# Kernel optimization log

Measured on AMD Instinct MI355X. Metric: run time of the kernel, lower is better.

The kernel has to match this reference:

```python
import jax, jax.numpy as jnp
import numpy as np

E, TOPK, HID, FFN = 8, 2, 1024, 2048  # experts, top_k, hidden K, intermediate N
B, S = 2, 1024


def setup_inputs() -> dict:
    key = jax.random.key(0)
    ks = jax.random.split(key, 7)
    return {
        "x": jax.random.normal(ks[0], (B, S, HID), jnp.float32),
        "router_weight": jax.random.normal(ks[1], (E, HID), jnp.float32) * 0.02,
        "router_bias": jax.random.normal(ks[2], (E,), jnp.float32) * 0.02,
        "w1": jax.random.normal(ks[3], (E, 2 * FFN, HID), jnp.float32) * 0.02,  # [E,2N,K] gate|up
        "w1_bias": jax.random.normal(ks[4], (E, 2 * FFN), jnp.float32) * 0.02,
        "w2": jax.random.normal(ks[5], (E, HID, FFN), jnp.float32) * 0.02,      # [E,K,N]
        "w2_bias": jax.random.normal(ks[6], (E, HID), jnp.float32) * 0.02,
        "top_k": TOPK,
    }


def reference(x, router_weight, router_bias, w1, w1_bias, w2, w2_bias, top_k):
    Bb, Ss, K = x.shape
    xf = x.reshape(-1, K)                                   # [M,K]
    M = xf.shape[0]
    Ne = w1.shape[0]
    # --- route_tokens: softmax over experts, then top-k (megablocks style) ---
    logits = xf @ router_weight.T + router_bias             # [M,E]
    probs = jax.nn.softmax(logits, axis=-1)
    topk_w, topk_ids = jax.lax.top_k(probs, top_k)          # [M,topk]
    # combine weights: scatter top-k probs into dense [M,E]
    comb = jnp.zeros((M, Ne), xf.dtype).at[jnp.arange(M)[:, None], topk_ids].add(topk_w)
    # --- fused experts (dense combine formulation, same math as grouped GEMM) ---
    gu = jnp.einsum('mk,enk->men', xf, w1) + w1_bias[None]  # [M,E,2N]
    Nf = gu.shape[-1] // 2
    gate, up = gu[..., :Nf], gu[..., Nf:]
    h = jax.nn.silu(gate) * up                              # silu_and_mul (SwiGLU)
    down = jnp.einsum('men,ekn->mek', h, w2) + w2_bias[None]  # [M,E,K]
    out = jnp.einsum('mek,me->mk', down, comb)              # weighted combine
    return out.reshape(Bb, Ss, K), topk_w
```

## Files before the change

kernel.cpp:

```cpp
#include <hip/hip_runtime.h>
#include <hip/hip_bf16.h>
#include <math.h>

#define E_    8
#define HID_  1024
#define FFN_  2048
#define M_    2048
#define NP_   (M_*2)

typedef __attribute__((ext_vector_type(8))) short bf16x8;
typedef __attribute__((ext_vector_type(8))) short short8v;
typedef __attribute__((ext_vector_type(4))) float f32x4;
typedef __attribute__((ext_vector_type(4))) int   i32x4;

typedef const __attribute__((address_space(1))) void GVOID;
typedef __attribute__((address_space(3))) void LVOID;

#define VMCNT4 asm volatile("s_waitcnt vmcnt(4)" ::: "memory")
#define VMCNT0 asm volatile("s_waitcnt vmcnt(0)" ::: "memory")

__device__ __forceinline__ short f2bf(float f) {
    union { __hip_bfloat16 b; short s; } u;
    u.b = __float2bfloat16(f);
    return u.s;
}

__device__ __forceinline__ bf16x8 pk8(f32x4 lo, f32x4 hi) {
    unsigned u0, u1, u2, u3;
    asm("v_cvt_pk_bf16_f32 %0, %1, %2" : "=v"(u0) : "v"(lo.x), "v"(lo.y));
    asm("v_cvt_pk_bf16_f32 %0, %1, %2" : "=v"(u1) : "v"(lo.z), "v"(lo.w));
    asm("v_cvt_pk_bf16_f32 %0, %1, %2" : "=v"(u2) : "v"(hi.x), "v"(hi.y));
    asm("v_cvt_pk_bf16_f32 %0, %1, %2" : "=v"(u3) : "v"(hi.z), "v"(hi.w));
    union { i32x4 i; bf16x8 b; } r;
    r.i = (i32x4){(int)u0, (int)u1, (int)u2, (int)u3};
    return r.b;
}

__global__ __launch_bounds__(64) void router_kernel(
    const float* __restrict__ x, const float* __restrict__ rw,
    const float* __restrict__ rb, int* __restrict__ ids,
    float* __restrict__ wts, int* __restrict__ cnt,
    float* __restrict__ topk_out, __hip_bfloat16* __restrict__ xb)
{
    const int m    = blockIdx.x;
    const int lane = threadIdx.x;
    const float4* xm4 = (const float4*)(x + (size_t)m * HID_);

    float4 xv[4];
#pragma unroll
    for (int j = 0; j < 4; ++j) xv[j] = xm4[j*64 + lane];

    short4* xbr = (short4*)(xb + (size_t)m * HID_);
#pragma unroll
    for (int j = 0; j < 4; ++j) {
        short4 o;
        o.x = f2bf(xv[j].x); o.y = f2bf(xv[j].y);
        o.z = f2bf(xv[j].z); o.w = f2bf(xv[j].w);
        xbr[j*64 + lane] = o;
    }

    float lg[E_];
#pragma unroll
    for (int e = 0; e < E_; ++e) {
        const float4* we4 = (const float4*)(rw + e * HID_);
        float s = 0.f;
#pragma unroll
        for (int j = 0; j < 4; ++j) {
            float4 w = we4[j*64 + lane];
            s = fmaf(xv[j].x, w.x, s);
            s = fmaf(xv[j].y, w.y, s);
            s = fmaf(xv[j].z, w.z, s);
            s = fmaf(xv[j].w, w.w, s);
        }
        lg[e] = s;
    }
#pragma unroll
    for (int off = 32; off; off >>= 1)
#pragma unroll
        for (int e = 0; e < E_; ++e) lg[e] += __shfl_xor(lg[e], off);

    if (lane == 0) {
        float l2[E_], p[E_];
        float mx = -1e30f;
#pragma unroll
        for (int e = 0; e < E_; ++e) { l2[e] = lg[e] + rb[e]; mx = fmaxf(mx, l2[e]); }
        float sum = 0.f;
#pragma unroll
        for (int e = 0; e < E_; ++e) { p[e] = expf(l2[e] - mx); sum += p[e]; }
        float inv = 1.f / sum;
#pragma unroll
        for (int e = 0; e < E_; ++e) p[e] *= inv;

        int   i1 = -1, i2 = -1;
        float v1 = -1e30f, v2 = -1e30f;
#pragma unroll
        for (int e = 0; e < E_; ++e) {
            float pe = p[e];
            if (pe > v1)      { v2 = v1; i2 = i1; v1 = pe; i1 = e; }
            else if (pe > v2) { v2 = pe; i2 = e; }
        }
        ids[2*m]   = i1;  ids[2*m+1]   = i2;
        wts[2*m]   = v1;  wts[2*m+1]   = v2;
        topk_out[2*m]   = v1;
        topk_out[2*m+1] = v2;
        atomicAdd(&cnt[i1], 1);
        atomicAdd(&cnt[i2], 1);
    }
}

__global__ void offsets_kernel(const int* __restrict__ cnt,
                               int* __restrict__ off, int* __restrict__ fill)
{
    if (threadIdx.x == 0 && blockIdx.x == 0) {
        int acc = 0;
        for (int e = 0; e < E_; ++e) { off[e] = acc; fill[e] = acc; acc += cnt[e]; }
    }
}

__global__ __launch_bounds__(256) void scatter_kernel(
    const int* __restrict__ ids, const float* __restrict__ wts,
    int* __restrict__ fill, int* __restrict__ gtok, float* __restrict__ gwt,
    int* __restrict__ pos)
{
    int m = blockIdx.x * 256 + threadIdx.x;
    if (m >= M_) return;
#pragma unroll
    for (int s = 0; s < 2; ++s) {
        int e = ids[2*m + s];
        int p = atomicAdd(&fill[e], 1);
        gtok[p] = m;
        gwt[p]  = wts[2*m + s];
        pos[2*m + s] = p;
    }
}

__global__ __launch_bounds__(256, 3) void gemm1_kernel(
    const __hip_bfloat16* __restrict__ xb, const float* __restrict__ w1,
    const float* __restrict__ w1b, const int* __restrict__ gtok,
    const int* __restrict__ cnt, const int* __restrict__ off,
    __hip_bfloat16* __restrict__ h,
    const float* __restrict__ w2, __hip_bfloat16* __restrict__ w2bf)
{
    if (blockIdx.z == 8) {
        int pb = blockIdx.x + 32 * blockIdx.y;
        const float4* src = (const float4*)w2;
        short8v* dst = (short8v*)w2bf;
        size_t cb0 = (size_t)pb * 4096;
        for (int it = 0; it < 4; ++it) {
            size_t cbase = cb0 + it*1024;
            float4 a[4], b[4];
#pragma unroll
            for (int u = 0; u < 4; ++u) {
                size_t c = cbase + u*256 + threadIdx.x;
                a[u] = src[2*c];
                b[u] = src[2*c + 1];
            }
#pragma unroll
            for (int u = 0; u < 4; ++u) {
                size_t c = cbase + u*256 + threadIdx.x;
                short8v o;
                o[0] = f2bf(a[u].x); o[1] = f2bf(a[u].y);
                o[2] = f2bf(a[u].z); o[3] = f2bf(a[u].w);
                o[4] = f2bf(b[u].x); o[5] = f2bf(b[u].y);
                o[6] = f2bf(b[u].z); o[7] = f2bf(b[u].w);
                dst[c] = o;
            }
        }
        return;
    }

    const int e  = blockIdx.z;
    const int ce = cnt[e];
    const int t0 = blockIdx.y * 128;
    if (t0 >= ce) return;
    const int n0   = blockIdx.x * 64;
    const int base = off[e];
    const float* w1e = w1 + (size_t)e * (2*FFN_) * HID_;

    __shared__ __align__(16) __hip_bfloat16 As[2][128*32];
    __shared__ __align__(16) float          Bsf[2][128*32];

    const int tid  = threadIdx.x;
    const int lane = tid & 63;
    const int wid  = tid >> 6;
    const int wm   = wid >> 1;
    const int wn   = wid & 1;
    const int cf   = lane >> 4;

    const __hip_bfloat16* asrc[2];
#pragma unroll
    for (int q = 0; q < 2; ++q) {
        int slot = q*256 + tid;
        int r = slot >> 2, p = slot & 3;
        int c = p ^ ((r >> 1) & 3);
        int rr  = min(t0 + r, ce - 1);
        asrc[q] = xb + (size_t)gtok[base + rr] * HID_ + c*8;
    }
    const float* bsrc[4];
#pragma unroll
    for (int q = 0; q < 4; ++q) {
        int slot = q*256 + tid;
        int r = slot >> 3, p = slot & 7;
        int c = p ^ (r & 7);
        int q2 = r >> 5, s = r & 31;
        int grow = (q2 & 1) ? (FFN_ + n0 + (q2>>1)*32 + s)
                            : (       n0 + (q2>>1)*32 + s);
        bsrc[q] = w1e + (size_t)grow * HID_ + c*4;
    }

    auto STAGE = [&](int b, int k0) {
#pragma unroll
        for (int q = 0; q < 2; ++q)
            __builtin_amdgcn_global_load_lds((GVOID*)(asrc[q] + k0),
                (LVOID*)(&As[b][(q*256 + wid*64)*8]), 16, 0, 0);
#pragma unroll
        for (int q = 0; q < 4; ++q)
            __builtin_amdgcn_global_load_lds((GVOID*)(bsrc[q] + k0),
                (LVOID*)(&Bsf[b][(q*256 + wid*64)*4]), 16, 0, 0);
    };

    f32x4 acc[4][4];
#pragma unroll
    for (int m = 0; m < 4; ++m)
#pragma unroll
        for (int n = 0; n < 4; ++n) acc[m][n] = (f32x4){0.f,0.f,0.f,0.f};

    auto COMPUTE = [&](int cb) {
        bf16x8 af[4], bfr[4];
#pragma unroll
        for (int m = 0; m < 4; ++m) {
            int r = wm*64 + m*16 + (lane & 15);
            int sw = cf ^ ((r >> 1) & 3);
            af[m] = *(bf16x8*)&As[cb][r*32 + sw*8];
        }
#pragma unroll
        for (int n = 0; n < 4; ++n) {
            int r = wn*64 + n*16 + (lane & 15);
            int p0 = (2*cf)     ^ (r & 7);
            int p1 = (2*cf + 1) ^ (r & 7);
            f32x4 lo = *(f32x4*)&Bsf[cb][r*32 + p0*4];
            f32x4 hi = *(f32x4*)&Bsf[cb][r*32 + p1*4];
            bfr[n] = pk8(lo, hi);
        }
        __builtin_amdgcn_s_setprio(1);
#pragma unroll
        for (int m = 0; m < 4; ++m)
#pragma unroll
            for (int n = 0; n < 4; ++n)
                acc[m][n] = __builtin_amdgcn_mfma_f32_16x16x32_bf16(
                    af[m], bfr[n], acc[m][n], 0, 0, 0);
        __builtin_amdgcn_s_setprio(0);
    };

    const int NT = HID_/32;
    STAGE(0, 0);
    __syncthreads();
    for (int t = 0; t < NT; ++t) {
        int cur = t & 1, nxt = cur ^ 1;
        if (t + 1 < NT) STAGE(nxt, (t+1)*32);
        COMPUTE(cur);
        __syncthreads();
    }

    const float* w1be = w1b + e*2*FFN_;
#pragma unroll
    for (int n = 0; n < 2; ++n) {
        int col = n0 + wn*32 + n*16 + (lane & 15);
        float bg = w1be[col];
        float bu = w1be[FFN_ + col];
#pragma unroll
        for (int m = 0; m < 4; ++m) {
            int rb2 = t0 + wm*64 + m*16 + (lane >> 4)*4;
#pragma unroll
            for (int i = 0; i < 4; ++i) {
                int t = rb2 + i;
                if (t < ce) {
                    float g = acc[m][n][i]   + bg;
                    float u = acc[m][n+2][i] + bu;
                    float hv = (g / (1.f + __expf(-g))) * u;
                    h[(size_t)(base + t)*FFN_ + col] = __float2bfloat16(hv);
                }
            }
        }
    }
}

__global__ __launch_bounds__(256, 3) void gemm2_kernel(
    const __hip_bfloat16* __restrict__ h, const __hip_bfloat16* __restrict__ w2bf,
    const float* __restrict__ w2b, const float* __restrict__ gwt,
    const int* __restrict__ cnt, const int* __restrict__ off,
    float* __restrict__ dpair)
{
    const int e  = blockIdx.z & 7;
    const int ks = blockIdx.z >> 3;
    const int ce = cnt[e];
    const int t0 = blockIdx.y * 128;
    if (t0 >= ce) return;
    const int n0    = blockIdx.x * 128;
    const int base  = off[e];
    const int kbase = ks * (FFN_/2);
    const __hip_bfloat16* w2e = w2bf + (size_t)e * HID_ * FFN_;

    __shared__ __align__(16) __hip_bfloat16 As[3][128*32];
    __shared__ __align__(16) __hip_bfloat16 Bs[3][128*32];

    const int tid  = threadIdx.x;
    const int lane = tid & 63;
    const int wid  = tid >> 6;
    const int wm   = wid >> 1;
    const int wn   = wid & 1;

    const __hip_bfloat16 *asrc[2], *bsrc[2];
#pragma unroll
    for (int q = 0; q < 2; ++q) {
        int slot = q*256 + tid;
        int r = slot >> 2, p = slot & 3;
        int c = p ^ ((r >> 1) & 3);
        int rr = min(t0 + r, ce - 1);
        asrc[q] = h   + (size_t)(base + rr) * FFN_ + kbase + c*8;
        bsrc[q] = w2e + (size_t)(n0 + r)    * FFN_ + kbase + c*8;
    }

    auto STAGE = [&](int b, int k0) {
#pragma unroll
        for (int q = 0; q < 2; ++q)
            __builtin_amdgcn_global_load_lds((GVOID*)(asrc[q] + k0),
                (LVOID*)(&As[b][(q*256 + wid*64)*8]), 16, 0, 0);
#pragma unroll
        for (int q = 0; q < 2; ++q)
            __builtin_amdgcn_global_load_lds((GVOID*)(bsrc[q] + k0),
                (LVOID*)(&Bs[b][(q*256 + wid*64)*8]), 16, 0, 0);
    };

    f32x4 acc[4][4];
#pragma unroll
    for (int m = 0; m < 4; ++m)
#pragma unroll
        for (int n = 0; n < 4; ++n) acc[m][n] = (f32x4){0.f,0.f,0.f,0.f};

    const int cf = lane >> 4;
    auto COMPUTE = [&](int cb) {
        bf16x8 af[4], bfr[4];
#pragma unroll
        for (int m = 0; m < 4; ++m) {
            int r = wm*64 + m*16 + (lane & 15);
            int sw = cf ^ ((r >> 1) & 3);
            af[m] = *(bf16x8*)&As[cb][r*32 + sw*8];
        }
#pragma unroll
        for (int n = 0; n < 4; ++n) {
            int r = wn*64 + n*16 + (lane & 15);
            int sw = cf ^ ((r >> 1) & 3);
            bfr[n] = *(bf16x8*)&Bs[cb][r*32 + sw*8];
        }
        __builtin_amdgcn_s_setprio(1);
#pragma unroll
        for (int m = 0; m < 4; ++m)
#pragma unroll
            for (int n = 0; n < 4; ++n)
                acc[m][n] = __builtin_amdgcn_mfma_f32_16x16x32_bf16(
                    af[m], bfr[n], acc[m][n], 0, 0, 0);
        __builtin_amdgcn_s_setprio(0);
    };

    const int NT = (FFN_/2)/32;
    STAGE(0, 0);
    STAGE(1, 32);
    VMCNT4;
    __builtin_amdgcn_s_barrier();

    int cb = 0;
    for (int t = 0; t < NT-2; ++t) {
        int sb = cb + 2; if (sb >= 3) sb -= 3;
        STAGE(sb, (t+2)*32);
        COMPUTE(cb);
        VMCNT4;
        __builtin_amdgcn_s_barrier();
        if (++cb == 3) cb = 0;
    }
    COMPUTE(cb);
    VMCNT0;
    __builtin_amdgcn_s_barrier();
    if (++cb == 3) cb = 0;
    COMPUTE(cb);

    const float* w2be = w2b + e*HID_;
    float* dpk = dpair + (size_t)ks * NP_ * HID_;
#pragma unroll
    for (int n = 0; n < 4; ++n) {
        int col = n0 + wn*64 + n*16 + (lane & 15);
        float bias = (ks == 0) ? w2be[col] : 0.f;
#pragma unroll
        for (int m = 0; m < 4; ++m) {
            int rb2 = t0 + wm*64 + m*16 + (lane >> 4)*4;
#pragma unroll
            for (int i = 0; i < 4; ++i) {
                int t = rb2 + i;
                if (t < ce) {
                    int p   = base + t;
                    float w = gwt[p];
                    dpk[(size_t)p*HID_ + col] = w * (acc[m][n][i] + bias);
                }
            }
        }
    }
}

__global__ __launch_bounds__(256) void combine_kernel(
    const float* __restrict__ dpair, const int* __restrict__ pos,
    float* __restrict__ out)
{
    int idx = blockIdx.x * 256 + threadIdx.x;
    int m   = idx >> 8;
    int c4  = (idx & 255) * 4;
    int p0 = pos[2*m], p1 = pos[2*m+1];
    const float* d0 = dpair;
    const float* d1 = dpair + (size_t)NP_ * HID_;
    float4 a0 = *(const float4*)(d0 + (size_t)p0*HID_ + c4);
    float4 a1 = *(const float4*)(d1 + (size_t)p0*HID_ + c4);
    float4 b0 = *(const float4*)(d0 + (size_t)p1*HID_ + c4);
    float4 b1 = *(const float4*)(d1 + (size_t)p1*HID_ + c4);
    float4 o = make_float4((a0.x+a1.x)+(b0.x+b1.x), (a0.y+a1.y)+(b0.y+b1.y),
                           (a0.z+a1.z)+(b0.z+b1.z), (a0.w+a1.w)+(b0.w+b1.w));
    *(float4*)(out + (size_t)m*HID_ + c4) = o;
}

__global__ __launch_bounds__(256) void gemm1_rs_kernel(
    const __hip_bfloat16* __restrict__ xb, const float* __restrict__ w1,
    const float* __restrict__ w1b, const int* __restrict__ gtok,
    const int* __restrict__ cnt, const int* __restrict__ off,
    __hip_bfloat16* __restrict__ h)
{
    const int e  = blockIdx.z;
    const int ce = cnt[e];
    const int t0 = blockIdx.y * 128;
    if (t0 >= ce) return;
    const int n0   = blockIdx.x * 64;
    const int base = off[e];
    const float* w1e = w1 + (size_t)e * (2*FFN_) * HID_;

    __shared__ __align__(16) __hip_bfloat16 As[128*64];
    __shared__ __align__(16) __hip_bfloat16 Bs[128*64];

    const int tid  = threadIdx.x;
    const int lane = tid & 63;
    const int wid  = tid >> 6;
    const int wm   = wid >> 1;
    const int wn   = wid & 1;

    const __hip_bfloat16* asrc[4];
#pragma unroll
    for (int q = 0; q < 4; ++q) {
        int slot = q*256 + tid;
        int r = slot >> 3, p = slot & 7;
        int rr  = min(t0 + r, ce - 1);
        int tok = gtok[base + rr];
        int c = p ^ (r & 7);
        asrc[q] = xb + (size_t)tok * HID_ + c*8;
    }

    const int brow = tid >> 1;
    const int hk   = tid & 1;
    const int q2 = brow >> 5, s = brow & 31;
    const int grow = (q2 & 1) ? (FFN_ + n0 + (q2>>1)*32 + s)
                              : (       n0 + (q2>>1)*32 + s);
    const float* bsrc = w1e + (size_t)grow * HID_ + hk*32;

    f32x4 acc[4][4];
#pragma unroll
    for (int m = 0; m < 4; ++m)
#pragma unroll
        for (int n = 0; n < 4; ++n) acc[m][n] = (f32x4){0.f,0.f,0.f,0.f};

    float4 breg[8];
#pragma unroll
    for (int j = 0; j < 8; ++j) breg[j] = *(const float4*)(bsrc + j*4);

    for (int k0 = 0; k0 < HID_; k0 += 64) {
#pragma unroll
        for (int q = 0; q < 4; ++q) {
            __builtin_amdgcn_global_load_lds(
                (GVOID*)(asrc[q] + k0),
                (LVOID*)(&As[(q*256 + wid*64)*8]), 16, 0, 0);
        }
#pragma unroll
        for (int cc = 0; cc < 4; ++cc) {
            union { bf16x8 v; short s8[8]; } u;
            const float* f0 = (const float*)&breg[2*cc];
#pragma unroll
            for (int j = 0; j < 8; ++j) u.s8[j] = f2bf(f0[j]);
            int c = hk*4 + cc, p = c ^ (brow & 7);
            *(bf16x8*)&Bs[brow*64 + p*8] = u.v;
        }
        __syncthreads();

        if (k0 + 64 < HID_) {
#pragma unroll
            for (int j = 0; j < 8; ++j) breg[j] = *(const float4*)(bsrc + (k0+64) + j*4);
        }

        bf16x8 af[4][2], bfr[4][2];
#pragma unroll
        for (int m = 0; m < 4; ++m)
#pragma unroll
            for (int kk = 0; kk < 2; ++kk) {
                int r = wm*64 + m*16 + (lane & 15);
                int c = kk*4 + (lane >> 4), p = c ^ (r & 7);
                af[m][kk] = *(bf16x8*)&As[r*64 + p*8];
            }
#pragma unroll
        for (int n = 0; n < 4; ++n)
#pragma unroll
            for (int kk = 0; kk < 2; ++kk) {
                int r = wn*64 + n*16 + (lane & 15);
                int c = kk*4 + (lane >> 4), p = c ^ (r & 7);
                bfr[n][kk] = *(bf16x8*)&Bs[r*64 + p*8];
            }
#pragma unroll
        for (int kk = 0; kk < 2; ++kk)
#pragma unroll
            for (int m = 0; m < 4; ++m)
#pragma unroll
                for (int n = 0; n < 4; ++n)
                    acc[m][n] = __builtin_amdgcn_mfma_f32_16x16x32_bf16(
                        af[m][kk], bfr[n][kk], acc[m][n], 0, 0, 0);
        __syncthreads();
    }

    const float* w1be = w1b + e*2*FFN_;
#pragma unroll
    for (int n = 0; n < 2; ++n) {
        int col = n0 + wn*32 + n*16 + (lane & 15);
        float bg = w1be[col];
        float bu = w1be[FFN_ + col];
#pragma unroll
        for (int m = 0; m < 4; ++m) {
            int rb2 = t0 + wm*64 + m*16 + (lane >> 4)*4;
#pragma unroll
            for (int i = 0; i < 4; ++i) {
                int t = rb2 + i;
                if (t < ce) {
                    float g = acc[m][n][i]   + bg;
                    float u = acc[m][n+2][i] + bu;
                    float hv = (g / (1.f + __expf(-g))) * u;
                    h[(size_t)(base + t)*FFN_ + col] = __float2bfloat16(hv);
                }
            }
        }
    }
}

__global__ __launch_bounds__(256) void gemm2_rs_kernel(
    const __hip_bfloat16* __restrict__ h, const float* __restrict__ w2,
    const float* __restrict__ w2b, const int* __restrict__ gtok,
    const float* __restrict__ gwt, const int* __restrict__ cnt,
    const int* __restrict__ off, float* __restrict__ out)
{
    const int e  = blockIdx.z;
    const int ce = cnt[e];
    const int t0 = blockIdx.y * 128;
    if (t0 >= ce) return;
    const int n0   = blockIdx.x * 128;
    const int base = off[e];
    const float* w2e = w2 + (size_t)e * HID_ * FFN_;

    __shared__ __align__(16) __hip_bfloat16 As[128*64];
    __shared__ __align__(16) __hip_bfloat16 Bs[128*64];

    const int tid  = threadIdx.x;
    const int lane = tid & 63;
    const int wid  = tid >> 6;
    const int wm   = wid >> 1;
    const int wn   = wid & 1;

    const __hip_bfloat16* asrc[4];
#pragma unroll
    for (int q = 0; q < 4; ++q) {
        int slot = q*256 + tid;
        int r = slot >> 3, p = slot & 7;
        int rr = min(t0 + r, ce - 1);
        int c = p ^ (r & 7);
        asrc[q] = h + (size_t)(base + rr) * FFN_ + c*8;
    }

    const int brow = tid >> 1;
    const int hk   = tid & 1;
    const float* bsrc = w2e + (size_t)(n0 + brow) * FFN_ + hk*32;

    f32x4 acc[4][4];
#pragma unroll
    for (int m = 0; m < 4; ++m)
#pragma unroll
        for (int n = 0; n < 4; ++n) acc[m][n] = (f32x4){0.f,0.f,0.f,0.f};

    float4 breg[8];
#pragma unroll
    for (int j = 0; j < 8; ++j) breg[j] = *(const float4*)(bsrc + j*4);

    for (int k0 = 0; k0 < FFN_; k0 += 64) {
#pragma unroll
        for (int q = 0; q < 4; ++q) {
            __builtin_amdgcn_global_load_lds(
                (GVOID*)(asrc[q] + k0),
                (LVOID*)(&As[(q*256 + wid*64)*8]), 16, 0, 0);
        }
#pragma unroll
        for (int cc = 0; cc < 4; ++cc) {
            union { bf16x8 v; short s8[8]; } u;
            const float* f0 = (const float*)&breg[2*cc];
#pragma unroll
            for (int j = 0; j < 8; ++j) u.s8[j] = f2bf(f0[j]);
            int c = hk*4 + cc, p = c ^ (brow & 7);
            *(bf16x8*)&Bs[brow*64 + p*8] = u.v;
        }
        __syncthreads();

        if (k0 + 64 < FFN_) {
#pragma unroll
            for (int j = 0; j < 8; ++j) breg[j] = *(const float4*)(bsrc + (k0+64) + j*4);
        }

        bf16x8 af[4][2], bfr[4][2];
#pragma unroll
        for (int m = 0; m < 4; ++m)
#pragma unroll
            for (int kk = 0; kk < 2; ++kk) {
                int r = wm*64 + m*16 + (lane & 15);
                int c = kk*4 + (lane >> 4), p = c ^ (r & 7);
                af[m][kk] = *(bf16x8*)&As[r*64 + p*8];
            }
#pragma unroll
        for (int n = 0; n < 4; ++n)
#pragma unroll
            for (int kk = 0; kk < 2; ++kk) {
                int r = wn*64 + n*16 + (lane & 15);
                int c = kk*4 + (lane >> 4), p = c ^ (r & 7);
                bfr[n][kk] = *(bf16x8*)&Bs[r*64 + p*8];
            }
#pragma unroll
        for (int kk = 0; kk < 2; ++kk)
#pragma unroll
            for (int m = 0; m < 4; ++m)
#pragma unroll
                for (int n = 0; n < 4; ++n)
                    acc[m][n] = __builtin_amdgcn_mfma_f32_16x16x32_bf16(
                        af[m][kk], bfr[n][kk], acc[m][n], 0, 0, 0);
        __syncthreads();
    }

    const float* w2be = w2b + e*HID_;
#pragma unroll
    for (int n = 0; n < 4; ++n) {
        int col = n0 + wn*64 + n*16 + (lane & 15);
        float bias = w2be[col];
#pragma unroll
        for (int m = 0; m < 4; ++m) {
            int rb2 = t0 + wm*64 + m*16 + (lane >> 4)*4;
#pragma unroll
            for (int i = 0; i < 4; ++i) {
                int t = rb2 + i;
                if (t < ce) {
                    int p   = base + t;
                    float w = gwt[p];
                    atomicAdd(&out[(size_t)gtok[p]*HID_ + col], w * (acc[m][n][i] + bias));
                }
            }
        }
    }
}

extern "C" void kernel_launch(void* const* d_in, const int* in_sizes, int n_in,
                              void* d_out, int out_size, void* d_ws, size_t ws_size,
                              hipStream_t stream)
{
    const float* x   = (const float*)d_in[0];
    const float* rw  = (const float*)d_in[1];
    const float* rb  = (const float*)d_in[2];
    const float* w1  = (const float*)d_in[3];
    const float* w1b = (const float*)d_in[4];
    const float* w2  = (const float*)d_in[5];
    const float* w2b = (const float*)d_in[6];

    float* out      = (float*)d_out;
    float* topk_out = out + (size_t)M_ * HID_;

    char*  ws   = (char*)d_ws;
    int*   ids  = (int*)  (ws);
    float* wts  = (float*)(ws + 16384);
    int*   gtok = (int*)  (ws + 32768);
    float* gwt  = (float*)(ws + 49152);
    int*   cnt  = (int*)  (ws + 65536);
    int*   off  = (int*)  (ws + 65536 + 128);
    int*   fill = (int*)  (ws + 65536 + 256);
    int*   pos  = (int*)  (ws + 98304);

    const size_t MB = 1024*1024;
    __hip_bfloat16* xb    = (__hip_bfloat16*)(ws + 131072);
    __hip_bfloat16* h     = (__hip_bfloat16*)(ws + 131072 + 4*MB);
    float*          dpair = (float*)         (ws + 131072 + 20*MB);
    __hip_bfloat16* w2bf  = (__hip_bfloat16*)(ws + 131072 + 52*MB);
    const bool tier2 = (ws_size >= 131072 + 84*MB);

    hipMemsetAsync(cnt, 0, E_ * sizeof(int), stream);

    router_kernel<<<M_, 64, 0, stream>>>(x, rw, rb, ids, wts, cnt, topk_out, xb);
    offsets_kernel<<<1, 64, 0, stream>>>(cnt, off, fill);
    scatter_kernel<<<M_/256, 256, 0, stream>>>(ids, wts, fill, gtok, gwt, pos);

    if (tier2) {
        dim3 g1(FFN_/64, M_/128, E_ + 1);
        gemm1_kernel<<<g1, 256, 0, stream>>>(xb, w1, w1b, gtok, cnt, off, h,
                                             w2, w2bf);

        dim3 g2(HID_/128, M_/128, 2*E_);
        gemm2_kernel<<<g2, 256, 0, stream>>>(h, w2bf, w2b, gwt, cnt, off, dpair);

        combine_kernel<<<(M_*HID_)/(256*4), 256, 0, stream>>>(dpair, pos, out);
    } else {
        hipMemsetAsync(out, 0, (size_t)M_ * HID_ * sizeof(float), stream);

        dim3 g1(FFN_/64, M_/128, E_);
        gemm1_rs_kernel<<<g1, 256, 0, stream>>>(xb, w1, w1b, gtok, cnt, off, h);

        dim3 g2(HID_/128, M_/128, E_);
        gemm2_rs_kernel<<<g2, 256, 0, stream>>>(h, w2, w2b, gtok, gwt, cnt, off, out);
    }
}
```

Baseline: 229.4 us.

## Use fixed per-expert slot regions and fuse token scatter into router

Each expert now gets a fixed region of M slots, so token positions are assigned directly in the router with atomics on per-expert fill counters. This removes the separate offsets and scatter kernels and their launch overhead. The cost is larger h and dpair buffers, indexed by expert*M, and a much higher workspace requirement for the fast tier2 path. If the workspace is too small, execution falls back to the slower path.

```diff
diff --git a/kernel.cpp b/kernel.cpp
--- a/kernel.cpp
+++ b/kernel.cpp
@@ -6,7 +6,7 @@
 #define HID_  1024
 #define FFN_  2048
 #define M_    2048
-#define NP_   (M_*2)
+#define NP2_  (E_*M_)
 
 typedef __attribute__((ext_vector_type(8))) short bf16x8;
 typedef __attribute__((ext_vector_type(8))) short short8v;
@@ -38,8 +38,8 @@
 
 __global__ __launch_bounds__(64) void router_kernel(
     const float* __restrict__ x, const float* __restrict__ rw,
-    const float* __restrict__ rb, int* __restrict__ ids,
-    float* __restrict__ wts, int* __restrict__ cnt,
+    const float* __restrict__ rb, int* __restrict__ fill,
+    int* __restrict__ gtok, float* __restrict__ gwt, int* __restrict__ pos,
     float* __restrict__ topk_out, __hip_bfloat16* __restrict__ xb)
 {
     const int m    = blockIdx.x;
@@ -99,46 +99,21 @@
             if (pe > v1)      { v2 = v1; i2 = i1; v1 = pe; i1 = e; }
             else if (pe > v2) { v2 = pe; i2 = e; }
         }
-        ids[2*m]   = i1;  ids[2*m+1]   = i2;
-        wts[2*m]   = v1;  wts[2*m+1]   = v2;
         topk_out[2*m]   = v1;
         topk_out[2*m+1] = v2;
-        atomicAdd(&cnt[i1], 1);
-        atomicAdd(&cnt[i2], 1);
-    }
-}
-
-__global__ void offsets_kernel(const int* __restrict__ cnt,
-                               int* __restrict__ off, int* __restrict__ fill)
-{
-    if (threadIdx.x == 0 && blockIdx.x == 0) {
-        int acc = 0;
-        for (int e = 0; e < E_; ++e) { off[e] = acc; fill[e] = acc; acc += cnt[e]; }
-    }
-}
-
-__global__ __launch_bounds__(256) void scatter_kernel(
-    const int* __restrict__ ids, const float* __restrict__ wts,
-    int* __restrict__ fill, int* __restrict__ gtok, float* __restrict__ gwt,
-    int* __restrict__ pos)
-{
-    int m = blockIdx.x * 256 + threadIdx.x;
-    if (m >= M_) return;
-#pragma unroll
-    for (int s = 0; s < 2; ++s) {
-        int e = ids[2*m + s];
-        int p = atomicAdd(&fill[e], 1);
-        gtok[p] = m;
-        gwt[p]  = wts[2*m + s];
-        pos[2*m + s] = p;
+        int p1s = atomicAdd(&fill[i1], 1);
+        int s1  = i1*M_ + p1s;
+        gtok[s1] = m; gwt[s1] = v1; pos[2*m]   = s1;
+        int p2s = atomicAdd(&fill[i2], 1);
+        int s2  = i2*M_ + p2s;
+        gtok[s2] = m; gwt[s2] = v2; pos[2*m+1] = s2;
     }
 }
 
 __global__ __launch_bounds__(256, 3) void gemm1_kernel(
     const __hip_bfloat16* __restrict__ xb, const float* __restrict__ w1,
     const float* __restrict__ w1b, const int* __restrict__ gtok,
-    const int* __restrict__ cnt, const int* __restrict__ off,
-    __hip_bfloat16* __restrict__ h,
+    const int* __restrict__ fill, __hip_bfloat16* __restrict__ h,
     const float* __restrict__ w2, __hip_bfloat16* __restrict__ w2bf)
 {
     if (blockIdx.z == 8) {
@@ -170,11 +145,11 @@
     }
 
     const int e  = blockIdx.z;
-    const int ce = cnt[e];
+    const int ce = fill[e];
     const int t0 = blockIdx.y * 128;
     if (t0 >= ce) return;
     const int n0   = blockIdx.x * 64;
-    const int base = off[e];
+    const int base = e * M_;
     const float* w1e = w1 + (size_t)e * (2*FFN_) * HID_;
 
     __shared__ __align__(16) __hip_bfloat16 As[2][128*32];
@@ -288,16 +263,15 @@
 __global__ __launch_bounds__(256, 3) void gemm2_kernel(
     const __hip_bfloat16* __restrict__ h, const __hip_bfloat16* __restrict__ w2bf,
     const float* __restrict__ w2b, const float* __restrict__ gwt,
-    const int* __restrict__ cnt, const int* __restrict__ off,
-    float* __restrict__ dpair)
+    const int* __restrict__ fill, float* __restrict__ dpair)
 {
     const int e  = blockIdx.z & 7;
     const int ks = blockIdx.z >> 3;
-    const int ce = cnt[e];
+    const int ce = fill[e];
     const int t0 = blockIdx.y * 128;
     if (t0 >= ce) return;
     const int n0    = blockIdx.x * 128;
-    const int base  = off[e];
+    const int base  = e * M_;
     const int kbase = ks * (FFN_/2);
     const __hip_bfloat16* w2e = w2bf + (size_t)e * HID_ * FFN_;
 
@@ -385,7 +359,7 @@
     COMPUTE(cb);
 
     const float* w2be = w2b + e*HID_;
-    float* dpk = dpair + (size_t)ks * NP_ * HID_;
+    float* dpk = dpair + (size_t)ks * NP2_ * HID_;
 #pragma unroll
     for (int n = 0; n < 4; ++n) {
         int col = n0 + wn*64 + n*16 + (lane & 15);
@@ -415,7 +389,7 @@
     int c4  = (idx & 255) * 4;
     int p0 = pos[2*m], p1 = pos[2*m+1];
     const float* d0 = dpair;
-    const float* d1 = dpair + (size_t)NP_ * HID_;
+    const float* d1 = dpair + (size_t)NP2_ * HID_;
     float4 a0 = *(const float4*)(d0 + (size_t)p0*HID_ + c4);
     float4 a1 = *(const float4*)(d1 + (size_t)p0*HID_ + c4);
     float4 b0 = *(const float4*)(d0 + (size_t)p1*HID_ + c4);
@@ -428,15 +402,14 @@
 __global__ __launch_bounds__(256) void gemm1_rs_kernel(
     const __hip_bfloat16* __restrict__ xb, const float* __restrict__ w1,
     const float* __restrict__ w1b, const int* __restrict__ gtok,
-    const int* __restrict__ cnt, const int* __restrict__ off,
-    __hip_bfloat16* __restrict__ h)
+    const int* __restrict__ fill, __hip_bfloat16* __restrict__ h)
 {
     const int e  = blockIdx.z;
-    const int ce = cnt[e];
+    const int ce = fill[e];
     const int t0 = blockIdx.y * 128;
     if (t0 >= ce) return;
     const int n0   = blockIdx.x * 64;
-    const int base = off[e];
+    const int base = e * M_;
     const float* w1e = w1 + (size_t)e * (2*FFN_) * HID_;
 
     __shared__ __align__(16) __hip_bfloat16 As[128*64];
@@ -553,15 +526,15 @@
 __global__ __launch_bounds__(256) void gemm2_rs_kernel(
     const __hip_bfloat16* __restrict__ h, const float* __restrict__ w2,
     const float* __restrict__ w2b, const int* __restrict__ gtok,
-    const float* __restrict__ gwt, const int* __restrict__ cnt,
-    const int* __restrict__ off, float* __restrict__ out)
+    const float* __restrict__ gwt, const int* __restrict__ fill,
+    float* __restrict__ out)
 {
     const int e  = blockIdx.z;
-    const int ce = cnt[e];
+    const int ce = fill[e];
     const int t0 = blockIdx.y * 128;
     if (t0 >= ce) return;
     const int n0   = blockIdx.x * 128;
-    const int base = off[e];
+    const int base = e * M_;
     const float* w2e = w2 + (size_t)e * HID_ * FFN_;
 
     __shared__ __align__(16) __hip_bfloat16 As[128*64];
@@ -684,45 +657,39 @@
     float* out      = (float*)d_out;
     float* topk_out = out + (size_t)M_ * HID_;
 
+    const size_t MB = 1024*1024;
     char*  ws   = (char*)d_ws;
-    int*   ids  = (int*)  (ws);
-    float* wts  = (float*)(ws + 16384);
-    int*   gtok = (int*)  (ws + 32768);
-    float* gwt  = (float*)(ws + 49152);
-    int*   cnt  = (int*)  (ws + 65536);
-    int*   off  = (int*)  (ws + 65536 + 128);
-    int*   fill = (int*)  (ws + 65536 + 256);
-    int*   pos  = (int*)  (ws + 98304);
-
-    const size_t MB = 1024*1024;
-    __hip_bfloat16* xb    = (__hip_bfloat16*)(ws + 131072);
-    __hip_bfloat16* h     = (__hip_bfloat16*)(ws + 131072 + 4*MB);
-    float*          dpair = (float*)         (ws + 131072 + 20*MB);
-    __hip_bfloat16* w2bf  = (__hip_bfloat16*)(ws + 131072 + 52*MB);
-    const bool tier2 = (ws_size >= 131072 + 84*MB);
-
-    hipMemsetAsync(cnt, 0, E_ * sizeof(int), stream);
-
-    router_kernel<<<M_, 64, 0, stream>>>(x, rw, rb, ids, wts, cnt, topk_out, xb);
-    offsets_kernel<<<1, 64, 0, stream>>>(cnt, off, fill);
-    scatter_kernel<<<M_/256, 256, 0, stream>>>(ids, wts, fill, gtok, gwt, pos);
+    int*   fill = (int*)  (ws);
+    int*   pos  = (int*)  (ws + 128);
+    int*   gtok = (int*)  (ws + 65536);
+    float* gwt  = (float*)(ws + 131072);
+    __hip_bfloat16* xb    = (__hip_bfloat16*)(ws + 1*MB);
+    __hip_bfloat16* h     = (__hip_bfloat16*)(ws + 5*MB);
+    float*          dpair = (float*)         (ws + 69*MB);
+    __hip_bfloat16* w2bf  = (__hip_bfloat16*)(ws + 197*MB);
+    const bool tier2 = (ws_size >= 230*MB);
+
+    hipMemsetAsync(fill, 0, E_ * sizeof(int), stream);
+
+    router_kernel<<<M_, 64, 0, stream>>>(x, rw, rb, fill, gtok, gwt, pos,
+                                         topk_out, xb);
 
     if (tier2) {
         dim3 g1(FFN_/64, M_/128, E_ + 1);
-        gemm1_kernel<<<g1, 256, 0, stream>>>(xb, w1, w1b, gtok, cnt, off, h,
+        gemm1_kernel<<<g1, 256, 0, stream>>>(xb, w1, w1b, gtok, fill, h,
                                              w2, w2bf);
 
         dim3 g2(HID_/128, M_/128, 2*E_);
-        gemm2_kernel<<<g2, 256, 0, stream>>>(h, w2bf, w2b, gwt, cnt, off, dpair);
+        gemm2_kernel<<<g2, 256, 0, stream>>>(h, w2bf, w2b, gwt, fill, dpair);
 
         combine_kernel<<<(M_*HID_)/(256*4), 256, 0, stream>>>(dpair, pos, out);
     } else {
         hipMemsetAsync(out, 0, (size_t)M_ * HID_ * sizeof(float), stream);
 
         dim3 g1(FFN_/64, M_/128, E_);
-        gemm1_rs_kernel<<<g1, 256, 0, stream>>>(xb, w1, w1b, gtok, cnt, off, h);
+        gemm1_rs_kernel<<<g1, 256, 0, stream>>>(xb, w1, w1b, gtok, fill, h);
 
         dim3 g2(HID_/128, M_/128, E_);
-        gemm2_rs_kernel<<<g2, 256, 0, stream>>>(h, w2, w2b, gtok, gwt, cnt, off, out);
-    }
-}
+        gemm2_rs_kernel<<<g2, 256, 0, stream>>>(h, w2, w2b, gtok, gwt, fill, out);
+    }
+}
```

New measurement: 211.4 us, median of 2. 7.9% less time.
